# Kernel tuning notes

Hardware: AMD Instinct MI355X
Metric: run time of the kernel (lower is better)

## Reference

```python
import jax, jax.numpy as jnp
import numpy as np

LOG2PI = float(np.log(2.0 * np.pi))
CLIP_LO, CLIP_HI = 1e-6, 1.0 - 1e-6


def gaussian_log_prob(X, mu):
    # X: (s, d), mu: (K, d) -> (s, K); unit-variance diagonal Normal.
    d = X.shape[-1]
    sq = (
        (X * X).sum(-1, keepdims=True)
        - 2.0 * (X @ mu.T)
        + (mu * mu).sum(-1)[None, :]
    )
    return -0.5 * (sq + d * LOG2PI)


def setup_inputs() -> dict:
    key = jax.random.key(0)
    kz, ks, kd, km1, km2 = jax.random.split(key, 5)
    s, K, n, dz = 60000, 200, 6, 64
    Z = jax.random.normal(kz, (s, dz), dtype=jnp.float32)
    S = jax.random.normal(ks, (s, 3), dtype=jnp.float32)
    D = jax.random.randint(kd, (s, n), 0, s, dtype=jnp.int64)
    sel_mu = jax.random.normal(km1, (K, dz), dtype=jnp.float32)
    spa_mu = jax.random.normal(km2, (K, 3), dtype=jnp.float32)
    return {"Z": Z, "S": S, "D": D, "sel_mu": sel_mu, "spa_mu": spa_mu}


def reference(Z, S, D, sel_mu, spa_mu):
    # point energy U: (s, K)
    U = -(gaussian_log_prob(Z, sel_mu) + gaussian_log_prob(S, spa_mu))
    Q = jax.nn.softmax(-U, axis=-1)  # temperature = 1.0
    # expected point energy: (s,)
    point = (Q * U).sum(-1)
    # doublet energy: gather neighbor rows, coassignment, potential, mask
    Qc = jnp.clip(Q, CLIP_LO, CLIP_HI)
    co = jnp.einsum('snk,sk->sn', Qc[D], Qc)  # (s, n)
    doublet = jnp.where(D < 0, 0.0, -jnp.log(co)).sum(-1)  # (s,)
    return point + doublet
```

## Files before the change

### kernel.cpp

```cpp
#include <hip/hip_runtime.h>
#include <hip/hip_fp16.h>
#include <math.h>

#define KK 200
#define NT 13
#define NNB 6
#define Q8STRIDE 256

typedef __attribute__((ext_vector_type(8))) short short8;
typedef __attribute__((ext_vector_type(4))) float f32x4;
#define MFMA16 __builtin_amdgcn_mfma_f32_16x16x32_bf16

__device__ __forceinline__ unsigned short bfh(float f) {
    unsigned u = __float_as_uint(f);
    return (unsigned short)((u + 0x7fffu + ((u >> 16) & 1u)) >> 16);
}
__device__ __forceinline__ float bf2f(unsigned short h) {
    return __uint_as_float(((unsigned)h) << 16);
}
__device__ __forceinline__ short8 z8() {
    short8 v;
#pragma unroll
    for (int j = 0; j < 8; ++j) v[j] = 0;
    return v;
}
__device__ __forceinline__ void cv2(float f, short8& hi, short8& lo, int j) {
    unsigned short h = bfh(f);
    hi[j] = (short)h;
    lo[j] = (short)bfh(f - bf2f(h));
}
__device__ __forceinline__ unsigned char f2e5(float f) {
    unsigned short hb = __half_as_ushort(__float2half(f));
    return (unsigned char)((hb + 0x7fu + ((hb >> 8) & 1u)) >> 8);
}
__device__ __forceinline__ void dec8(unsigned w, float* f) {
    f[0] = __half2float(__ushort_as_half((unsigned short)((w << 8) & 0xff00u)));
    f[1] = __half2float(__ushort_as_half((unsigned short)(w & 0xff00u)));
    f[2] = __half2float(__ushort_as_half((unsigned short)((w >> 8) & 0xff00u)));
    f[3] = __half2float(__ushort_as_half((unsigned short)((w >> 16) & 0xff00u)));
}

__global__ __launch_bounds__(512, 4) void
k_point(const float* __restrict__ Z, const float* __restrict__ S,
        const float* __restrict__ selmu, const float* __restrict__ spamu,
        unsigned short* __restrict__ Qcb, unsigned char* __restrict__ Qc8,
        float* __restrict__ pointbuf, int sRows, int mTiles)
{
    __shared__ short8 ldsBh[26 * 64];
    __shared__ short8 ldsBl[26 * 64];
    __shared__ uint2  ldsB2h[NT * 16];
    __shared__ uint2  ldsB2l[NT * 16];

    const int tid = threadIdx.x;

    for (int slot = tid; slot < 26 * 64; slot += 512) {
        int L = slot & 63, ts = slot >> 6;
        int t = ts >> 1, sstep = ts & 1;
        int n = t * 16 + (L & 15);
        int kb = sstep * 32 + (L >> 4) * 8;
        short8 hi = z8(), lo = z8();
        if (n < KK) {
            const float* mp = selmu + (size_t)n * 64 + kb;
            float4 a = *(const float4*)mp;
            float4 b = *(const float4*)(mp + 4);
            cv2(a.x, hi, lo, 0); cv2(a.y, hi, lo, 1); cv2(a.z, hi, lo, 2); cv2(a.w, hi, lo, 3);
            cv2(b.x, hi, lo, 4); cv2(b.y, hi, lo, 5); cv2(b.z, hi, lo, 6); cv2(b.w, hi, lo, 7);
        }
        ldsBh[slot] = hi;
        ldsBl[slot] = lo;
    }
    if (tid < NT * 16) {
        int n = tid;
        uint2 vh = make_uint2(0, 0), vl = make_uint2(0, 0);
        if (n < KK) {
            float p0 = spamu[n * 3 + 0], p1 = spamu[n * 3 + 1], p2 = spamu[n * 3 + 2];
            float nrm = p0 * p0 + p1 * p1 + p2 * p2;
            const float* mp = selmu + (size_t)n * 64;
#pragma unroll 8
            for (int k = 0; k < 64; ++k) { float m = mp[k]; nrm = fmaf(m, m, nrm); }
            nrm *= -0.5f;
            unsigned short h0 = bfh(p0), h1 = bfh(p1), h2 = bfh(p2), h3 = bfh(nrm);
            unsigned short g0 = bfh(p0 - bf2f(h0)), g1 = bfh(p1 - bf2f(h1));
            unsigned short g2 = bfh(p2 - bf2f(h2)), g3 = bfh(nrm - bf2f(h3));
            vh = make_uint2((unsigned)h0 | ((unsigned)h1 << 16), (unsigned)h2 | ((unsigned)h3 << 16));
            vl = make_uint2((unsigned)g0 | ((unsigned)g1 << 16), (unsigned)g2 | ((unsigned)g3 << 16));
        }
        ldsB2h[tid] = vh;
        ldsB2l[tid] = vl;
    }
    __syncthreads();

    const int lane = tid & 63;
    const int q = lane >> 4;
    const int li = lane & 15;

    const float cLog = 0.5f * 67.0f * 1.8378770664093453f;

    for (int wg = blockIdx.x * 8 + (tid >> 6); wg < mTiles; wg += gridDim.x * 8) {
        const int m0 = wg * 16;
        const int rowA = (m0 + li < sRows) ? (m0 + li) : (sRows - 1);

        const float* zr = Z + (size_t)rowA * 64 + q * 8;
        float4 z0 = *(const float4*)zr;
        float4 z1 = *(const float4*)(zr + 4);
        float4 z2 = *(const float4*)(zr + 32);
        float4 z3 = *(const float4*)(zr + 36);
        short8 ah0 = z8(), al0 = z8(), ah1 = z8(), al1 = z8();
        cv2(z0.x, ah0, al0, 0); cv2(z0.y, ah0, al0, 1); cv2(z0.z, ah0, al0, 2); cv2(z0.w, ah0, al0, 3);
        cv2(z1.x, ah0, al0, 4); cv2(z1.y, ah0, al0, 5); cv2(z1.z, ah0, al0, 6); cv2(z1.w, ah0, al0, 7);
        cv2(z2.x, ah1, al1, 0); cv2(z2.y, ah1, al1, 1); cv2(z2.z, ah1, al1, 2); cv2(z2.w, ah1, al1, 3);
        cv2(z3.x, ah1, al1, 4); cv2(z3.y, ah1, al1, 5); cv2(z3.z, ah1, al1, 6); cv2(z3.w, ah1, al1, 7);

        float zz = z0.x*z0.x + z0.y*z0.y + z0.z*z0.z + z0.w*z0.w
                 + z1.x*z1.x + z1.y*z1.y + z1.z*z1.z + z1.w*z1.w
                 + z2.x*z2.x + z2.y*z2.y + z2.z*z2.z + z2.w*z2.w
                 + z3.x*z3.x + z3.y*z3.y + z3.z*z3.z + z3.w*z3.w;
        zz += __shfl_xor(zz, 16);
        zz += __shfl_xor(zz, 32);

        float s0v = S[(size_t)rowA * 3 + 0];
        float s1v = S[(size_t)rowA * 3 + 1];
        float s2v = S[(size_t)rowA * 3 + 2];
        float cz = 0.5f * (zz + s0v * s0v + s1v * s1v + s2v * s2v) + cLog;

        short8 a2h = z8(), a2l = z8();
        if (lane < 16) {
            cv2(s0v, a2h, a2l, 0);
            cv2(s1v, a2h, a2l, 1);
            cv2(s2v, a2h, a2l, 2);
            a2h[3] = (short)bfh(1.0f);
        }

        f32x4 acc[NT];
#pragma unroll
        for (int t = 0; t < NT; ++t) { f32x4 zv = {0.f, 0.f, 0.f, 0.f}; acc[t] = zv; }

#pragma unroll
        for (int t = 0; t < NT; ++t) {
            short8 b0 = ldsBh[(t * 2 + 0) * 64 + lane];
            short8 b1 = ldsBh[(t * 2 + 1) * 64 + lane];
            short8 c0 = ldsBl[(t * 2 + 0) * 64 + lane];
            short8 c1 = ldsBl[(t * 2 + 1) * 64 + lane];
            uint2 bh2 = make_uint2(0, 0), bl2 = make_uint2(0, 0);
            if (lane < 16) { bh2 = ldsB2h[t * 16 + lane]; bl2 = ldsB2l[t * 16 + lane]; }
            short8 B2h = z8(), B2l = z8();
            B2h[0] = (short)(bh2.x & 0xffff); B2h[1] = (short)(bh2.x >> 16);
            B2h[2] = (short)(bh2.y & 0xffff); B2h[3] = (short)(bh2.y >> 16);
            B2l[0] = (short)(bl2.x & 0xffff); B2l[1] = (short)(bl2.x >> 16);
            B2l[2] = (short)(bl2.y & 0xffff); B2l[3] = (short)(bl2.y >> 16);

            acc[t] = MFMA16(ah0, b0, acc[t], 0, 0, 0);
            acc[t] = MFMA16(ah1, b1, acc[t], 0, 0, 0);
            acc[t] = MFMA16(al0, b0, acc[t], 0, 0, 0);
            acc[t] = MFMA16(al1, b1, acc[t], 0, 0, 0);
            acc[t] = MFMA16(ah0, c0, acc[t], 0, 0, 0);
            acc[t] = MFMA16(ah1, c1, acc[t], 0, 0, 0);
            acc[t] = MFMA16(a2h, B2h, acc[t], 0, 0, 0);
            acc[t] = MFMA16(a2l, B2h, acc[t], 0, 0, 0);
            acc[t] = MFMA16(a2h, B2l, acc[t], 0, 0, 0);
        }

#pragma unroll
        for (int r = 0; r < 4; ++r) {
            const int row = m0 + q * 4 + r;
            float e[NT];
            float mx = -1e30f;
#pragma unroll
            for (int t = 0; t < NT; ++t) {
                float v = acc[t][r];
                if (t == 12 && li >= 8) v = -1e30f;
                e[t] = v;
                mx = fmaxf(mx, v);
            }
            mx = fmaxf(mx, __shfl_xor(mx, 1));
            mx = fmaxf(mx, __shfl_xor(mx, 2));
            mx = fmaxf(mx, __shfl_xor(mx, 4));
            mx = fmaxf(mx, __shfl_xor(mx, 8));
            float sl = 0.f, pl = 0.f;
#pragma unroll
            for (int t = 0; t < NT; ++t) {
                float v = e[t];
                float ee = __expf(v - mx);
                sl += ee;
                pl = fmaf(ee, v, pl);
                e[t] = ee;
            }
#pragma unroll
            for (int off = 1; off <= 8; off <<= 1) {
                sl += __shfl_xor(sl, off);
                pl += __shfl_xor(pl, off);
            }
            float inv = 1.0f / sl;
            if (row < sRows) {
#pragma unroll
                for (int t = 0; t < NT; ++t) {
                    if (t < 12 || li < 8) {
                        float qv = fminf(fmaxf(e[t] * inv, 1e-6f), 1.0f - 1e-6f);
                        Qcb[(size_t)row * KK + t * 16 + li] = bfh(qv);
                        Qc8[(size_t)row * Q8STRIDE + t * 16 + li] = f2e5(qv * 1024.0f);
                    }
                }
                float czr = __shfl(cz, q * 4 + r);
                if (li == 0) pointbuf[row] = czr - pl * inv;
            }
        }
    }
}

__global__ __launch_bounds__(512) void
k_doublet(const unsigned short* __restrict__ Qcb, const unsigned char* __restrict__ Qc8,
          const float* __restrict__ pointbuf, const int* __restrict__ D,
          float* __restrict__ out, int sRows, int mTiles)
{
    const int wave = threadIdx.x >> 6;
    const int lane = threadIdx.x & 63;
    const int half = lane >> 5;
    const int l = lane & 31;
    const int sub = blockIdx.x >> 9;
    const int b = blockIdx.x & 511;
    const int T = b * 8 + wave;
    if (T >= mTiles) return;
    const int rbase = T * 16 + sub * 8;

    const bool act = (l < 25);
    const int lc = act ? l : 0;
    const float LN1024 = 6.93147180559945f;

    int   row  = rbase + half;
    int   rowc = (row < sRows) ? row : (sRows - 1);
    uint4 own  = *(const uint4*)(Qcb + (size_t)rowc * KK + lc * 8);
    int   dj[NNB];
    uint2 nb[NNB];
#pragma unroll
    for (int j = 0; j < NNB; ++j) dj[j] = D[(size_t)rowc * NNB + j];
#pragma unroll
    for (int j = 0; j < NNB; ++j) {
        int dd = (dj[j] >= 0) ? dj[j] : rowc;
        nb[j] = *(const uint2*)(Qc8 + (size_t)dd * Q8STRIDE + lc * 8);
    }

    for (int it = 0; it < 4; ++it) {
        int   rowN = 0, rowcN = 0;
        uint4 ownN = make_uint4(0, 0, 0, 0);
        int   djN[NNB];
        uint2 nbN[NNB];
        if (it < 3) {
            rowN  = rbase + (it + 1) * 2 + half;
            rowcN = (rowN < sRows) ? rowN : (sRows - 1);
            ownN  = *(const uint4*)(Qcb + (size_t)rowcN * KK + lc * 8);
#pragma unroll
            for (int j = 0; j < NNB; ++j) djN[j] = D[(size_t)rowcN * NNB + j];
#pragma unroll
            for (int j = 0; j < NNB; ++j) {
                int dd = (djN[j] >= 0) ? djN[j] : rowcN;
                nbN[j] = *(const uint2*)(Qc8 + (size_t)dd * Q8STRIDE + lc * 8);
            }
        }

        float o[8];
        o[0] = bf2f((unsigned short)(own.x & 0xffff)); o[1] = bf2f((unsigned short)(own.x >> 16));
        o[2] = bf2f((unsigned short)(own.y & 0xffff)); o[3] = bf2f((unsigned short)(own.y >> 16));
        o[4] = bf2f((unsigned short)(own.z & 0xffff)); o[5] = bf2f((unsigned short)(own.z >> 16));
        o[6] = bf2f((unsigned short)(own.w & 0xffff)); o[7] = bf2f((unsigned short)(own.w >> 16));

        float pj[NNB];
#pragma unroll
        for (int j = 0; j < NNB; ++j) {
            float bv[8];
            dec8(nb[j].x, bv);
            dec8(nb[j].y, bv + 4);
            float t = o[0] * bv[0];
            t = fmaf(o[1], bv[1], t); t = fmaf(o[2], bv[2], t); t = fmaf(o[3], bv[3], t);
            t = fmaf(o[4], bv[4], t); t = fmaf(o[5], bv[5], t); t = fmaf(o[6], bv[6], t);
            t = fmaf(o[7], bv[7], t);
            pj[j] = act ? t : 0.f;
        }
#pragma unroll
        for (int off = 1; off <= 16; off <<= 1) {
#pragma unroll
            for (int j = 0; j < NNB; ++j) pj[j] += __shfl_xor(pj[j], off);
        }
        float dbl = 0.f;
#pragma unroll
        for (int j = 0; j < NNB; ++j)
            if (dj[j] >= 0) dbl += LN1024 - __logf(pj[j]);

        if (l == 0 && row < sRows) out[row] = pointbuf[row] + dbl;

        row = rowN; rowc = rowcN; own = ownN;
#pragma unroll
        for (int j = 0; j < NNB; ++j) { dj[j] = djN[j]; nb[j] = nbN[j]; }
    }
}

extern "C" void kernel_launch(void* const* d_in, const int* in_sizes, int n_in,
                              void* d_out, int out_size, void* d_ws, size_t ws_size,
                              hipStream_t stream) {
    const float* Z     = (const float*)d_in[0];
    const float* S     = (const float*)d_in[1];
    const int*   D     = (const int*)d_in[2];
    const float* selmu = (const float*)d_in[3];
    const float* spamu = (const float*)d_in[4];
    float* out = (float*)d_out;
    const int s = out_size;

    const size_t qcbB = (size_t)s * KK * 2;
    const size_t qc8B = (size_t)s * Q8STRIDE;
    unsigned short* Qcb = (unsigned short*)d_ws;
    unsigned char*  Qc8 = (unsigned char*)d_ws + qcbB;
    float* pointbuf = (float*)((char*)d_ws + qcbB + qc8B);

    const int mTiles = (s + 15) / 16;
    const int grid1 = (mTiles + 7) / 8;
    k_point<<<grid1, 512, 0, stream>>>(Z, S, selmu, spamu, Qcb, Qc8, pointbuf, s, mTiles);

    k_doublet<<<1024, 512, 0, stream>>>(Qcb, Qc8, pointbuf, D, out, s, mTiles);
}
```

Baseline: 111.3 us.

## Drop bf16 Q copy, use fp8 own rows, transpose MFMA for packed stores

Removes the bf16 Q buffer entirely and reads the row's own probabilities from the fp8 (e5m2-style) buffer too, cutting write and read traffic. The MFMA operands are swapped so each lane holds four consecutive clusters of one row, allowing packed 32-bit stores and a cheaper softmax reduction across quads. The doublet kernel adds a deeper prefetch pipeline for neighbor indices and own rows. The own-row values lose precision (fp8 instead of bf16), which raises rounding error in the coassignment log.

```diff
diff --git a/kernel.cpp b/kernel.cpp
--- a/kernel.cpp
+++ b/kernel.cpp
@@ -29,9 +29,9 @@
     hi[j] = (short)h;
     lo[j] = (short)bfh(f - bf2f(h));
 }
-__device__ __forceinline__ unsigned char f2e5(float f) {
+__device__ __forceinline__ unsigned f2e5(float f) {
     unsigned short hb = __half_as_ushort(__float2half(f));
-    return (unsigned char)((hb + 0x7fu + ((hb >> 8) & 1u)) >> 8);
+    return (unsigned)((unsigned short)((hb + 0x7fu + ((hb >> 8) & 1u)) >> 8));
 }
 __device__ __forceinline__ void dec8(unsigned w, float* f) {
     f[0] = __half2float(__ushort_as_half((unsigned short)((w << 8) & 0xff00u)));
@@ -43,8 +43,8 @@
 __global__ __launch_bounds__(512, 4) void
 k_point(const float* __restrict__ Z, const float* __restrict__ S,
         const float* __restrict__ selmu, const float* __restrict__ spamu,
-        unsigned short* __restrict__ Qcb, unsigned char* __restrict__ Qc8,
-        float* __restrict__ pointbuf, int sRows, int mTiles)
+        unsigned char* __restrict__ Qc8, float* __restrict__ pointbuf,
+        int sRows, int mTiles)
 {
     __shared__ short8 ldsBh[26 * 64];
     __shared__ short8 ldsBl[26 * 64];
@@ -90,127 +90,132 @@
     }
     __syncthreads();
 
+    const int wave = tid >> 6;
     const int lane = tid & 63;
     const int q = lane >> 4;
     const int li = lane & 15;
-
     const float cLog = 0.5f * 67.0f * 1.8378770664093453f;
 
-    for (int wg = blockIdx.x * 8 + (tid >> 6); wg < mTiles; wg += gridDim.x * 8) {
-        const int m0 = wg * 16;
-        const int rowA = (m0 + li < sRows) ? (m0 + li) : (sRows - 1);
-
-        const float* zr = Z + (size_t)rowA * 64 + q * 8;
-        float4 z0 = *(const float4*)zr;
-        float4 z1 = *(const float4*)(zr + 4);
-        float4 z2 = *(const float4*)(zr + 32);
-        float4 z3 = *(const float4*)(zr + 36);
-        short8 ah0 = z8(), al0 = z8(), ah1 = z8(), al1 = z8();
-        cv2(z0.x, ah0, al0, 0); cv2(z0.y, ah0, al0, 1); cv2(z0.z, ah0, al0, 2); cv2(z0.w, ah0, al0, 3);
-        cv2(z1.x, ah0, al0, 4); cv2(z1.y, ah0, al0, 5); cv2(z1.z, ah0, al0, 6); cv2(z1.w, ah0, al0, 7);
-        cv2(z2.x, ah1, al1, 0); cv2(z2.y, ah1, al1, 1); cv2(z2.z, ah1, al1, 2); cv2(z2.w, ah1, al1, 3);
-        cv2(z3.x, ah1, al1, 4); cv2(z3.y, ah1, al1, 5); cv2(z3.z, ah1, al1, 6); cv2(z3.w, ah1, al1, 7);
-
-        float zz = z0.x*z0.x + z0.y*z0.y + z0.z*z0.z + z0.w*z0.w
-                 + z1.x*z1.x + z1.y*z1.y + z1.z*z1.z + z1.w*z1.w
-                 + z2.x*z2.x + z2.y*z2.y + z2.z*z2.z + z2.w*z2.w
-                 + z3.x*z3.x + z3.y*z3.y + z3.z*z3.z + z3.w*z3.w;
-        zz += __shfl_xor(zz, 16);
-        zz += __shfl_xor(zz, 32);
-
-        float s0v = S[(size_t)rowA * 3 + 0];
-        float s1v = S[(size_t)rowA * 3 + 1];
-        float s2v = S[(size_t)rowA * 3 + 2];
-        float cz = 0.5f * (zz + s0v * s0v + s1v * s1v + s2v * s2v) + cLog;
-
-        short8 a2h = z8(), a2l = z8();
-        if (lane < 16) {
-            cv2(s0v, a2h, a2l, 0);
-            cv2(s1v, a2h, a2l, 1);
-            cv2(s2v, a2h, a2l, 2);
-            a2h[3] = (short)bfh(1.0f);
-        }
-
-        f32x4 acc[NT];
-#pragma unroll
-        for (int t = 0; t < NT; ++t) { f32x4 zv = {0.f, 0.f, 0.f, 0.f}; acc[t] = zv; }
-
+    const int tile = blockIdx.x * 8 + wave;
+    if (tile >= mTiles) return;
+    const int m0 = tile * 16;
+    const int row = m0 + li;
+    const int rowA = (row < sRows) ? row : (sRows - 1);
+
+    const float* zr = Z + (size_t)rowA * 64 + q * 8;
+    float4 z0 = *(const float4*)zr;
+    float4 z1 = *(const float4*)(zr + 4);
+    float4 z2 = *(const float4*)(zr + 32);
+    float4 z3 = *(const float4*)(zr + 36);
+    short8 ah0 = z8(), al0 = z8(), ah1 = z8(), al1 = z8();
+    cv2(z0.x, ah0, al0, 0); cv2(z0.y, ah0, al0, 1); cv2(z0.z, ah0, al0, 2); cv2(z0.w, ah0, al0, 3);
+    cv2(z1.x, ah0, al0, 4); cv2(z1.y, ah0, al0, 5); cv2(z1.z, ah0, al0, 6); cv2(z1.w, ah0, al0, 7);
+    cv2(z2.x, ah1, al1, 0); cv2(z2.y, ah1, al1, 1); cv2(z2.z, ah1, al1, 2); cv2(z2.w, ah1, al1, 3);
+    cv2(z3.x, ah1, al1, 4); cv2(z3.y, ah1, al1, 5); cv2(z3.z, ah1, al1, 6); cv2(z3.w, ah1, al1, 7);
+
+    float zz = z0.x*z0.x + z0.y*z0.y + z0.z*z0.z + z0.w*z0.w
+             + z1.x*z1.x + z1.y*z1.y + z1.z*z1.z + z1.w*z1.w
+             + z2.x*z2.x + z2.y*z2.y + z2.z*z2.z + z2.w*z2.w
+             + z3.x*z3.x + z3.y*z3.y + z3.z*z3.z + z3.w*z3.w;
+    zz += __shfl_xor(zz, 16);
+    zz += __shfl_xor(zz, 32);
+
+    float s0v = S[(size_t)rowA * 3 + 0];
+    float s1v = S[(size_t)rowA * 3 + 1];
+    float s2v = S[(size_t)rowA * 3 + 2];
+    float cz = 0.5f * (zz + s0v * s0v + s1v * s1v + s2v * s2v) + cLog;
+
+    short8 rsh = z8(), rsl = z8();
+    if (lane < 16) {
+        cv2(s0v, rsh, rsl, 0);
+        cv2(s1v, rsh, rsl, 1);
+        cv2(s2v, rsh, rsl, 2);
+        rsh[3] = (short)bfh(1.0f);
+    }
+
+    f32x4 acc[NT];
+#pragma unroll
+    for (int t = 0; t < NT; ++t) { f32x4 zv = {0.f, 0.f, 0.f, 0.f}; acc[t] = zv; }
+
+#pragma unroll
+    for (int t = 0; t < NT; ++t) {
+        short8 b0 = ldsBh[(t * 2 + 0) * 64 + lane];
+        short8 b1 = ldsBh[(t * 2 + 1) * 64 + lane];
+        short8 c0 = ldsBl[(t * 2 + 0) * 64 + lane];
+        short8 c1 = ldsBl[(t * 2 + 1) * 64 + lane];
+        uint2 bh2 = make_uint2(0, 0), bl2 = make_uint2(0, 0);
+        if (lane < 16) { bh2 = ldsB2h[t * 16 + lane]; bl2 = ldsB2l[t * 16 + lane]; }
+        short8 cmh = z8(), cml = z8();
+        cmh[0] = (short)(bh2.x & 0xffff); cmh[1] = (short)(bh2.x >> 16);
+        cmh[2] = (short)(bh2.y & 0xffff); cmh[3] = (short)(bh2.y >> 16);
+        cml[0] = (short)(bl2.x & 0xffff); cml[1] = (short)(bl2.x >> 16);
+        cml[2] = (short)(bl2.y & 0xffff); cml[3] = (short)(bl2.y >> 16);
+
+        acc[t] = MFMA16(b0, ah0, acc[t], 0, 0, 0);
+        acc[t] = MFMA16(b1, ah1, acc[t], 0, 0, 0);
+        acc[t] = MFMA16(b0, al0, acc[t], 0, 0, 0);
+        acc[t] = MFMA16(b1, al1, acc[t], 0, 0, 0);
+        acc[t] = MFMA16(c0, ah0, acc[t], 0, 0, 0);
+        acc[t] = MFMA16(c1, ah1, acc[t], 0, 0, 0);
+        acc[t] = MFMA16(cmh, rsh, acc[t], 0, 0, 0);
+        acc[t] = MFMA16(cmh, rsl, acc[t], 0, 0, 0);
+        acc[t] = MFMA16(cml, rsh, acc[t], 0, 0, 0);
+    }
+
+    const bool padQ = (q >= 2);
+    float mx = -1e30f;
+#pragma unroll
+    for (int t = 0; t < NT; ++t) {
+#pragma unroll
+        for (int r = 0; r < 4; ++r) {
+            float v = acc[t][r];
+            if (t == 12 && padQ) v = -1e30f;
+            acc[t][r] = v;
+            mx = fmaxf(mx, v);
+        }
+    }
+    mx = fmaxf(mx, __shfl_xor(mx, 16));
+    mx = fmaxf(mx, __shfl_xor(mx, 32));
+    float sl = 0.f, pl = 0.f;
+#pragma unroll
+    for (int t = 0; t < NT; ++t) {
+#pragma unroll
+        for (int r = 0; r < 4; ++r) {
+            float v = acc[t][r];
+            float ee = __expf(v - mx);
+            sl += ee;
+            pl = fmaf(ee, v, pl);
+            acc[t][r] = ee;
+        }
+    }
+    sl += __shfl_xor(sl, 16);
+    sl += __shfl_xor(sl, 32);
+    pl += __shfl_xor(pl, 16);
+    pl += __shfl_xor(pl, 32);
+    float inv = 1.0f / sl;
+
+    if (row < sRows) {
+        unsigned char* qp = Qc8 + (size_t)row * Q8STRIDE + q * 4;
 #pragma unroll
         for (int t = 0; t < NT; ++t) {
-            short8 b0 = ldsBh[(t * 2 + 0) * 64 + lane];
-            short8 b1 = ldsBh[(t * 2 + 1) * 64 + lane];
-            short8 c0 = ldsBl[(t * 2 + 0) * 64 + lane];
-            short8 c1 = ldsBl[(t * 2 + 1) * 64 + lane];
-            uint2 bh2 = make_uint2(0, 0), bl2 = make_uint2(0, 0);
-            if (lane < 16) { bh2 = ldsB2h[t * 16 + lane]; bl2 = ldsB2l[t * 16 + lane]; }
-            short8 B2h = z8(), B2l = z8();
-            B2h[0] = (short)(bh2.x & 0xffff); B2h[1] = (short)(bh2.x >> 16);
-            B2h[2] = (short)(bh2.y & 0xffff); B2h[3] = (short)(bh2.y >> 16);
-            B2l[0] = (short)(bl2.x & 0xffff); B2l[1] = (short)(bl2.x >> 16);
-            B2l[2] = (short)(bl2.y & 0xffff); B2l[3] = (short)(bl2.y >> 16);
-
-            acc[t] = MFMA16(ah0, b0, acc[t], 0, 0, 0);
-            acc[t] = MFMA16(ah1, b1, acc[t], 0, 0, 0);
-            acc[t] = MFMA16(al0, b0, acc[t], 0, 0, 0);
-            acc[t] = MFMA16(al1, b1, acc[t], 0, 0, 0);
-            acc[t] = MFMA16(ah0, c0, acc[t], 0, 0, 0);
-            acc[t] = MFMA16(ah1, c1, acc[t], 0, 0, 0);
-            acc[t] = MFMA16(a2h, B2h, acc[t], 0, 0, 0);
-            acc[t] = MFMA16(a2l, B2h, acc[t], 0, 0, 0);
-            acc[t] = MFMA16(a2h, B2l, acc[t], 0, 0, 0);
-        }
-
-#pragma unroll
-        for (int r = 0; r < 4; ++r) {
-            const int row = m0 + q * 4 + r;
-            float e[NT];
-            float mx = -1e30f;
-#pragma unroll
-            for (int t = 0; t < NT; ++t) {
-                float v = acc[t][r];
-                if (t == 12 && li >= 8) v = -1e30f;
-                e[t] = v;
-                mx = fmaxf(mx, v);
+            unsigned w = 0;
+            if (t < 12 || !padQ) {
+                float q0 = fminf(fmaxf(acc[t][0] * inv, 1e-6f), 1.0f - 1e-6f);
+                float q1 = fminf(fmaxf(acc[t][1] * inv, 1e-6f), 1.0f - 1e-6f);
+                float q2 = fminf(fmaxf(acc[t][2] * inv, 1e-6f), 1.0f - 1e-6f);
+                float q3 = fminf(fmaxf(acc[t][3] * inv, 1e-6f), 1.0f - 1e-6f);
+                w = f2e5(q0 * 1024.0f) | (f2e5(q1 * 1024.0f) << 8)
+                  | (f2e5(q2 * 1024.0f) << 16) | (f2e5(q3 * 1024.0f) << 24);
             }
-            mx = fmaxf(mx, __shfl_xor(mx, 1));
-            mx = fmaxf(mx, __shfl_xor(mx, 2));
-            mx = fmaxf(mx, __shfl_xor(mx, 4));
-            mx = fmaxf(mx, __shfl_xor(mx, 8));
-            float sl = 0.f, pl = 0.f;
-#pragma unroll
-            for (int t = 0; t < NT; ++t) {
-                float v = e[t];
-                float ee = __expf(v - mx);
-                sl += ee;
-                pl = fmaf(ee, v, pl);
-                e[t] = ee;
-            }
-#pragma unroll
-            for (int off = 1; off <= 8; off <<= 1) {
-                sl += __shfl_xor(sl, off);
-                pl += __shfl_xor(pl, off);
-            }
-            float inv = 1.0f / sl;
-            if (row < sRows) {
-#pragma unroll
-                for (int t = 0; t < NT; ++t) {
-                    if (t < 12 || li < 8) {
-                        float qv = fminf(fmaxf(e[t] * inv, 1e-6f), 1.0f - 1e-6f);
-                        Qcb[(size_t)row * KK + t * 16 + li] = bfh(qv);
-                        Qc8[(size_t)row * Q8STRIDE + t * 16 + li] = f2e5(qv * 1024.0f);
-                    }
-                }
-                float czr = __shfl(cz, q * 4 + r);
-                if (li == 0) pointbuf[row] = czr - pl * inv;
-            }
-        }
+            *(unsigned*)(qp + t * 16) = w;
+        }
+        if (lane < 16) pointbuf[row] = cz - pl * inv;
     }
 }
 
 __global__ __launch_bounds__(512) void
-k_doublet(const unsigned short* __restrict__ Qcb, const unsigned char* __restrict__ Qc8,
-          const float* __restrict__ pointbuf, const int* __restrict__ D,
-          float* __restrict__ out, int sRows, int mTiles)
+k_doublet(const unsigned char* __restrict__ Qc8, const float* __restrict__ pointbuf,
+          const int* __restrict__ D, float* __restrict__ out, int sRows, int mTiles)
 {
     const int wave = threadIdx.x >> 6;
     const int lane = threadIdx.x & 63;
@@ -220,55 +225,58 @@
     const int b = blockIdx.x & 511;
     const int T = b * 8 + wave;
     if (T >= mTiles) return;
-    const int rbase = T * 16 + sub * 8;
+    const int rbase = T * 16 + sub * 8 + half;
 
     const bool act = (l < 25);
     const int lc = act ? l : 0;
-    const float LN1024 = 6.93147180559945f;
-
-    int   row  = rbase + half;
-    int   rowc = (row < sRows) ? row : (sRows - 1);
-    uint4 own  = *(const uint4*)(Qcb + (size_t)rowc * KK + lc * 8);
-    int   dj[NNB];
-    uint2 nb[NNB];
-#pragma unroll
-    for (int j = 0; j < NNB; ++j) dj[j] = D[(size_t)rowc * NNB + j];
-#pragma unroll
-    for (int j = 0; j < NNB; ++j) {
-        int dd = (dj[j] >= 0) ? dj[j] : rowc;
-        nb[j] = *(const uint2*)(Qc8 + (size_t)dd * Q8STRIDE + lc * 8);
+    const float LN2_20 = 13.862943611198906f;
+
+    int   dj0[NNB], dj1[NNB], dj2[NNB];
+    uint2 nb0[NNB], nb1[NNB];
+    uint2 ow0, ow1;
+    {
+        int rc0 = rbase,     c0 = (rc0 < sRows) ? rc0 : (sRows - 1);
+        int rc1 = rbase + 2, c1 = (rc1 < sRows) ? rc1 : (sRows - 1);
+#pragma unroll
+        for (int j = 0; j < NNB; ++j) dj0[j] = D[(size_t)c0 * NNB + j];
+#pragma unroll
+        for (int j = 0; j < NNB; ++j) dj1[j] = D[(size_t)c1 * NNB + j];
+        ow0 = *(const uint2*)(Qc8 + (size_t)c0 * Q8STRIDE + lc * 8);
+        ow1 = *(const uint2*)(Qc8 + (size_t)c1 * Q8STRIDE + lc * 8);
+#pragma unroll
+        for (int j = 0; j < NNB; ++j) {
+            int dd = (dj0[j] >= 0) ? dj0[j] : c0;
+            nb0[j] = *(const uint2*)(Qc8 + (size_t)dd * Q8STRIDE + lc * 8);
+        }
     }
 
     for (int it = 0; it < 4; ++it) {
-        int   rowN = 0, rowcN = 0;
-        uint4 ownN = make_uint4(0, 0, 0, 0);
-        int   djN[NNB];
-        uint2 nbN[NNB];
+        const int row = rbase + it * 2;
+        if (it < 2) {
+            int rc = rbase + (it + 2) * 2;
+            int cc = (rc < sRows) ? rc : (sRows - 1);
+#pragma unroll
+            for (int j = 0; j < NNB; ++j) dj2[j] = D[(size_t)cc * NNB + j];
+        }
         if (it < 3) {
-            rowN  = rbase + (it + 1) * 2 + half;
-            rowcN = (rowN < sRows) ? rowN : (sRows - 1);
-            ownN  = *(const uint4*)(Qcb + (size_t)rowcN * KK + lc * 8);
-#pragma unroll
-            for (int j = 0; j < NNB; ++j) djN[j] = D[(size_t)rowcN * NNB + j];
+            int rc = rbase + (it + 1) * 2;
+            int cc = (rc < sRows) ? rc : (sRows - 1);
 #pragma unroll
             for (int j = 0; j < NNB; ++j) {
-                int dd = (djN[j] >= 0) ? djN[j] : rowcN;
-                nbN[j] = *(const uint2*)(Qc8 + (size_t)dd * Q8STRIDE + lc * 8);
+                int dd = (dj1[j] >= 0) ? dj1[j] : cc;
+                nb1[j] = *(const uint2*)(Qc8 + (size_t)dd * Q8STRIDE + lc * 8);
             }
         }
 
         float o[8];
-        o[0] = bf2f((unsigned short)(own.x & 0xffff)); o[1] = bf2f((unsigned short)(own.x >> 16));
-        o[2] = bf2f((unsigned short)(own.y & 0xffff)); o[3] = bf2f((unsigned short)(own.y >> 16));
-        o[4] = bf2f((unsigned short)(own.z & 0xffff)); o[5] = bf2f((unsigned short)(own.z >> 16));
-        o[6] = bf2f((unsigned short)(own.w & 0xffff)); o[7] = bf2f((unsigned short)(own.w >> 16));
-
+        dec8(ow0.x, o);
+        dec8(ow0.y, o + 4);
         float pj[NNB];
 #pragma unroll
         for (int j = 0; j < NNB; ++j) {
             float bv[8];
-            dec8(nb[j].x, bv);
-            dec8(nb[j].y, bv + 4);
+            dec8(nb0[j].x, bv);
+            dec8(nb0[j].y, bv + 4);
             float t = o[0] * bv[0];
             t = fmaf(o[1], bv[1], t); t = fmaf(o[2], bv[2], t); t = fmaf(o[3], bv[3], t);
             t = fmaf(o[4], bv[4], t); t = fmaf(o[5], bv[5], t); t = fmaf(o[6], bv[6], t);
@@ -283,13 +291,18 @@
         float dbl = 0.f;
 #pragma unroll
         for (int j = 0; j < NNB; ++j)
-            if (dj[j] >= 0) dbl += LN1024 - __logf(pj[j]);
+            if (dj0[j] >= 0) dbl += LN2_20 - __logf(pj[j]);
 
         if (l == 0 && row < sRows) out[row] = pointbuf[row] + dbl;
 
-        row = rowN; rowc = rowcN; own = ownN;
-#pragma unroll
-        for (int j = 0; j < NNB; ++j) { dj[j] = djN[j]; nb[j] = nbN[j]; }
+        ow0 = ow1;
+        if (it < 2) {
+            int rc = rbase + (it + 2) * 2;
+            int cc = (rc < sRows) ? rc : (sRows - 1);
+            ow1 = *(const uint2*)(Qc8 + (size_t)cc * Q8STRIDE + lc * 8);
+        }
+#pragma unroll
+        for (int j = 0; j < NNB; ++j) { dj0[j] = dj1[j]; dj1[j] = dj2[j]; nb0[j] = nb1[j]; }
     }
 }
 
@@ -304,15 +317,12 @@
     float* out = (float*)d_out;
     const int s = out_size;
 
-    const size_t qcbB = (size_t)s * KK * 2;
-    const size_t qc8B = (size_t)s * Q8STRIDE;
-    unsigned short* Qcb = (unsigned short*)d_ws;
-    unsigned char*  Qc8 = (unsigned char*)d_ws + qcbB;
-    float* pointbuf = (float*)((char*)d_ws + qcbB + qc8B);
+    unsigned char* Qc8 = (unsigned char*)d_ws;
+    float* pointbuf = (float*)((char*)d_ws + (size_t)s * Q8STRIDE);
 
     const int mTiles = (s + 15) / 16;
     const int grid1 = (mTiles + 7) / 8;
-    k_point<<<grid1, 512, 0, stream>>>(Z, S, selmu, spamu, Qcb, Qc8, pointbuf, s, mTiles);
-
-    k_doublet<<<1024, 512, 0, stream>>>(Qcb, Qc8, pointbuf, D, out, s, mTiles);
-}
+    k_point<<<grid1, 512, 0, stream>>>(Z, S, selmu, spamu, Qc8, pointbuf, s, mTiles);
+
+    k_doublet<<<1024, 512, 0, stream>>>(Qc8, pointbuf, D, out, s, mTiles);
+}
```

New measurement: 108.0 us. 1.03x faster.
